# Kernel optimization log

Measured on AMD Instinct MI355X. Metric: run time of the kernel, lower is better.

The kernel has to match this reference:

```python
import jax, jax.numpy as jnp
import numpy as np

B, T, DIM, S, DFF = 4, 2048, 2048, 4, 8192
SINKHORN_ITERS = 10


def setup_inputs() -> dict:
    key = jax.random.key(0)
    ks = jax.random.split(key, 12)

    def lin(k, fan_in, shape):
        bound = 1.0 / np.sqrt(fan_in)
        return jax.random.uniform(k, shape, jnp.float32, -bound, bound)

    return {
        "x": jax.random.normal(ks[0], (B, T, DIM), jnp.float32),
        # phi_* linears act on the S-times tiled vector of size S*DIM
        "phi_pre_w": lin(ks[1], S * DIM, (S, S * DIM)),
        "phi_pre_b": lin(ks[2], S * DIM, (S,)),
        "phi_post_w": lin(ks[3], S * DIM, (S, S * DIM)),
        "phi_post_b": lin(ks[4], S * DIM, (S,)),
        "phi_res_w": lin(ks[5], S * DIM, (S * S, S * DIM)),
        "phi_res_b": lin(ks[6], S * DIM, (S * S,)),
        "alpha_pre": jnp.ones((1,), jnp.float32),
        "alpha_post": jnp.ones((1,), jnp.float32),
        "alpha_res": jnp.ones((1,), jnp.float32),
        "b_pre": jnp.zeros((S,), jnp.float32),
        "b_post": jnp.zeros((S,), jnp.float32),
        "b_res": jnp.zeros((S, S), jnp.float32),
        # block = transformer MLP
        "W1": lin(ks[7], DIM, (DIM, DFF)),
        "b1": lin(ks[8], DIM, (DFF,)),
        "W2": lin(ks[9], DFF, (DFF, DIM)),
        "b2": lin(ks[10], DFF, (DIM,)),
    }


def sinkhorn_knopp(logits):
    # logits: [B, T, S, S] -> doubly-stochastic via exp + alternating normalization
    M = jnp.exp(logits)
    for _ in range(SINKHORN_ITERS):
        M = M / jnp.sum(M, axis=-1, keepdims=True)  # rows
        M = M / jnp.sum(M, axis=-2, keepdims=True)  # cols
    return M


def reference(x, phi_pre_w, phi_pre_b, phi_post_w, phi_post_b, phi_res_w,
              phi_res_b, alpha_pre, alpha_post, alpha_res, b_pre, b_post,
              b_res, W1, b1, W2, b2):
    bs, seq, d = x.shape
    s = b_pre.shape[0]
    eps = jnp.asarray(jnp.finfo(x.dtype).eps, x.dtype)
    # x_l = x expanded over S identical streams; x_vec = tile(x, S).
    # RMS over the tiled S*d vector == RMS over d (streams are copies).
    x_n = x * jax.lax.rsqrt(jnp.mean(x * x, axis=-1, keepdims=True) + eps)
    # Linear on the tiled vector == sum of the S weight blocks applied to x_n.
    Wp = phi_pre_w.reshape(s, s, d).sum(axis=1)        # [S, d]
    Wq = phi_post_w.reshape(s, s, d).sum(axis=1)       # [S, d]
    Wr = phi_res_w.reshape(s * s, s, d).sum(axis=1)    # [S*S, d]
    h_pre_t = alpha_pre * (jnp.einsum('btd,sd->bts', x_n, Wp) + phi_pre_b) + b_pre
    h_post_t = alpha_post * (jnp.einsum('btd,sd->bts', x_n, Wq) + phi_post_b) + b_post
    h_res_t = alpha_res * (jnp.einsum('btd,kd->btk', x_n, Wr) + phi_res_b)
    h_res_t = h_res_t.reshape(bs, seq, s, s) + b_res
    h_pre = jax.nn.sigmoid(h_pre_t)                    # [B,T,S]
    h_post = 2.0 * jax.nn.sigmoid(h_post_t)            # [B,T,S]
    h_res = sinkhorn_knopp(h_res_t)                    # [B,T,S,S]
    # block_input = sum_j x_l[:,:,j] * h_pre[...,j] ; streams identical -> x * sum_j h_pre
    block_input = x * jnp.sum(h_pre, axis=-1, keepdims=True)
    # block: MLP with exact (erf) GELU, matching torch default
    h = jax.nn.gelu(jnp.einsum('btd,df->btf', block_input, W1) + b1, approximate=False)
    block_out = jnp.einsum('btf,fd->btd', h, W2) + b2
    # out = sum_i [ (h_res @ x_l)_i + h_post_i * block_out ]
    #     = x * sum_{ij} h_res[ij] + block_out * sum_i h_post_i
    res_mix = jnp.sum(h_res, axis=(-2, -1))[..., None]         # [B,T,1]
    post_mix = jnp.sum(h_post, axis=-1, keepdims=True)          # [B,T,1]
    return x * res_mix + block_out * post_mix
```

## Files before the change

kernel.cpp:

```cpp
#include <hip/hip_runtime.h>
#include <hip/hip_bf16.h>
#include <cstdint>
#include <cstddef>

#define DIM   2048
#define DFF   8192
#define NROWS 8192
#define NFOLD 24

typedef float f32x4 __attribute__((ext_vector_type(4)));
typedef __bf16 bf16x8 __attribute__((ext_vector_type(8)));

__device__ __forceinline__ float sigmoidf_(float v) { return 1.0f / (1.0f + expf(-v)); }

__device__ __forceinline__ unsigned short f2bf(float v) {
    union { __hip_bfloat16 h; unsigned short u; } cv;
    cv.h = __float2bfloat16(v);
    return cv.u;
}

__device__ __forceinline__ void async_copy16(const void* g, void* l) {
    __builtin_amdgcn_global_load_lds((const __attribute__((address_space(1))) void*)g,
                                     (__attribute__((address_space(3))) void*)l, 16, 0, 0);
}

__device__ __forceinline__ void wg_barrier() {
    asm volatile("" ::: "memory");
    __builtin_amdgcn_s_barrier();
    asm volatile("" ::: "memory");
}

#define VM(n) asm volatile("s_waitcnt vmcnt(" #n ")" ::: "memory")
#define LGKM0 asm volatile("s_waitcnt lgkmcnt(0)" ::: "memory")

__global__ __launch_bounds__(256) void fold_kernel(const float* __restrict__ pre_w,
                                                   const float* __restrict__ post_w,
                                                   const float* __restrict__ res_w,
                                                   float* __restrict__ Wfold) {
    int idx = blockIdx.x * 256 + threadIdx.x;
    if (idx >= NFOLD * DIM) return;
    int r = idx >> 11;
    int d = idx & (DIM - 1);
    const float* src;
    if (r < 4)      src = pre_w  + (size_t)r * (4 * DIM);
    else if (r < 8) src = post_w + (size_t)(r - 4) * (4 * DIM);
    else            src = res_w  + (size_t)(r - 8) * (4 * DIM);
    Wfold[idx] = src[d] + src[DIM + d] + src[2 * DIM + d] + src[3 * DIM + d];
}

__global__ __launch_bounds__(256) void transpose_to_bf16(const float* __restrict__ in,
                                                         __hip_bfloat16* __restrict__ out,
                                                         int R, int C) {
    __shared__ float tile[32][33];
    int bx = blockIdx.x, by = blockIdx.y;
    int tx = threadIdx.x & 31, ty0 = threadIdx.x >> 5;
#pragma unroll
    for (int i = 0; i < 4; i++) {
        int ty = ty0 + i * 8;
        tile[ty][tx] = in[(size_t)(by * 32 + ty) * C + bx * 32 + tx];
    }
    __syncthreads();
#pragma unroll
    for (int i = 0; i < 4; i++) {
        int ty = ty0 + i * 8;
        out[(size_t)(bx * 32 + ty) * R + by * 32 + tx] = __float2bfloat16(tile[tx][ty]);
    }
}

__global__ __launch_bounds__(512) void gating_kernel(
    const float* __restrict__ x, const float* __restrict__ Wfold,
    const float* __restrict__ phi_pre_b, const float* __restrict__ phi_post_b,
    const float* __restrict__ phi_res_b,
    const float* __restrict__ alpha_pre, const float* __restrict__ alpha_post,
    const float* __restrict__ alpha_res,
    const float* __restrict__ b_pre, const float* __restrict__ b_post,
    const float* __restrict__ b_res,
    __hip_bfloat16* __restrict__ Abuf,
    float* __restrict__ g_res_arr, float* __restrict__ g_post_arr) {
    const int tid = threadIdx.x;
    const int lane = tid & 63, wave = tid >> 6;
    const int row = blockIdx.x * 8 + wave;

    const float4* x4 = (const float4*)x + (size_t)row * 512;
    const float4* w4 = (const float4*)Wfold;

    float4 xv[8];
#pragma unroll
    for (int j = 0; j < 8; j++) xv[j] = x4[j * 64 + lane];

    float p[25];
    p[24] = 0.f;
#pragma unroll
    for (int j = 0; j < 8; j++)
        p[24] += xv[j].x * xv[j].x + xv[j].y * xv[j].y + xv[j].z * xv[j].z + xv[j].w * xv[j].w;

    for (int r = 0; r < NFOLD; r++) {
        float acc = 0.f;
#pragma unroll
        for (int j = 0; j < 8; j++) {
            float4 wv = w4[r * 512 + j * 64 + lane];
            acc += xv[j].x * wv.x + xv[j].y * wv.y + xv[j].z * wv.z + xv[j].w * wv.w;
        }
        p[r] = acc;
    }

#pragma unroll
    for (int r = 0; r < 25; r++) {
        float v = p[r];
#pragma unroll
        for (int off = 1; off < 64; off <<= 1) v += __shfl_xor(v, off, 64);
        p[r] = v;
    }

    const float rms = rsqrtf(p[24] / (float)DIM + 1.1920928955078125e-07f);
    const float ap = alpha_pre[0], aq = alpha_post[0], ar = alpha_res[0];
    float gpre = 0.f, gpost = 0.f;
#pragma unroll
    for (int s = 0; s < 4; s++) {
        gpre  += sigmoidf_(ap * (rms * p[s]     + phi_pre_b[s])  + b_pre[s]);
        gpost += 2.0f * sigmoidf_(aq * (rms * p[4 + s] + phi_post_b[s]) + b_post[s]);
    }
    float Mm[4][4];
#pragma unroll
    for (int i = 0; i < 4; i++)
#pragma unroll
        for (int j = 0; j < 4; j++) {
            int k = i * 4 + j;
            Mm[i][j] = expf(ar * (rms * p[8 + k] + phi_res_b[k]) + b_res[k]);
        }
    for (int it = 0; it < 10; ++it) {
#pragma unroll
        for (int i = 0; i < 4; i++) {
            float rs = 1.0f / (Mm[i][0] + Mm[i][1] + Mm[i][2] + Mm[i][3]);
#pragma unroll
            for (int j = 0; j < 4; j++) Mm[i][j] *= rs;
        }
#pragma unroll
        for (int j = 0; j < 4; j++) {
            float cs = 1.0f / (Mm[0][j] + Mm[1][j] + Mm[2][j] + Mm[3][j]);
#pragma unroll
            for (int i = 0; i < 4; i++) Mm[i][j] *= cs;
        }
    }
    float gres = 0.f;
#pragma unroll
    for (int i = 0; i < 4; i++)
#pragma unroll
        for (int j = 0; j < 4; j++) gres += Mm[i][j];

    __hip_bfloat16* arow = Abuf + (size_t)row * DIM;
#pragma unroll
    for (int j = 0; j < 8; j++) {
        ushort4 u;
        u.x = f2bf(xv[j].x * gpre); u.y = f2bf(xv[j].y * gpre);
        u.z = f2bf(xv[j].z * gpre); u.w = f2bf(xv[j].w * gpre);
        *reinterpret_cast<ushort4*>(arow + (j * 64 + lane) * 4) = u;
    }
    if (lane == 0) {
        g_res_arr[row]  = gres;
        g_post_arr[row] = gpost;
    }
}

#define RD_A0                                                                     \
    _Pragma("unroll") for (int m = 0; m < 4; ++m) {                               \
        a0[m][0] = *(const bf16x8*)(A0r + baseA + m * 2048 + cb0);                \
        a0[m][1] = *(const bf16x8*)(A0r + baseA + m * 2048 + cb1);                \
    }
#define RD_A1                                                                     \
    _Pragma("unroll") for (int m = 0; m < 4; ++m) {                               \
        a1[m][0] = *(const bf16x8*)(A1r + baseA + m * 2048 + cb0);                \
        a1[m][1] = *(const bf16x8*)(A1r + baseA + m * 2048 + cb1);                \
    }
#define RD_B0                                                                     \
    _Pragma("unroll") for (int n = 0; n < 2; ++n) {                               \
        b0[n][0] = *(const bf16x8*)(B0r + baseB + n * 2048 + cb0);                \
        b0[n][1] = *(const bf16x8*)(B0r + baseB + n * 2048 + cb1);                \
    }
#define RD_B1                                                                     \
    _Pragma("unroll") for (int n = 0; n < 2; ++n) {                               \
        b1[n][0] = *(const bf16x8*)(B1r + baseB + n * 2048 + cb0);                \
        b1[n][1] = *(const bf16x8*)(B1r + baseB + n * 2048 + cb1);                \
    }

#define MQ(AF, BF, MO, NO)                                                        \
    __builtin_amdgcn_s_setprio(1);                                                \
    _Pragma("unroll") for (int m = 0; m < 4; ++m)                                 \
    _Pragma("unroll") for (int n = 0; n < 2; ++n) {                               \
        acc[(MO) + m][(NO) + n] = __builtin_amdgcn_mfma_f32_16x16x32_bf16(        \
            AF[m][0], BF[n][0], acc[(MO) + m][(NO) + n], 0, 0, 0);                \
        acc[(MO) + m][(NO) + n] = __builtin_amdgcn_mfma_f32_16x16x32_bf16(        \
            AF[m][1], BF[n][1], acc[(MO) + m][(NO) + n], 0, 0, 0);                \
    }                                                                             \
    __builtin_amdgcn_s_setprio(0);

#define STG_A(t_, h_)                                                             \
    if ((t_) < nk) {                                                              \
        char* l_ = ldsA + (((t_) & 1) * 32768) + (h_) * 16384 + wave * 1024;      \
        async_copy16(Ab + aOff[0][h_] + (size_t)(t_) * 128, l_);                  \
        async_copy16(Ab + aOff[1][h_] + (size_t)(t_) * 128, l_ + 8192);           \
    }
#define STG_B(t_, h_)                                                             \
    if ((t_) < nk) {                                                              \
        char* l_ = ldsB + (((t_) & 1) * 32768) + (h_) * 16384 + wave * 1024;      \
        async_copy16(Bb + bOff[0][h_] + (size_t)(t_) * 128, l_);                  \
        async_copy16(Bb + bOff[1][h_] + (size_t)(t_) * 128, l_ + 8192);           \
    }

template <int MODE, int NB>
__global__ __launch_bounds__(512, 2) void gemm256(
    const __hip_bfloat16* __restrict__ A, const __hip_bfloat16* __restrict__ Bt,
    int M, int N, int K, const float* __restrict__ bias,
    __hip_bfloat16* __restrict__ outh, float* __restrict__ outf,
    const float* __restrict__ x, const float* __restrict__ g_res,
    const float* __restrict__ g_post) {
    __shared__ __align__(16) char ldsA[65536];
    __shared__ __align__(16) char ldsB[65536];

    const int wg = blockIdx.x;
    const int xcd = wg & 7;
    const int i = wg >> 3;
    const int nt = xcd * NB + (i % NB);
    const int mt = i / NB;
    const int m0 = mt * 256;
    const int n0 = nt * 256;

    const int tid = threadIdx.x;
    const int lane = tid & 63;
    const int wave = tid >> 6;
    const int wr = wave >> 2;
    const int wc = wave & 3;
    const int q = lane >> 4;
    const int rr = lane & 7;

    const uint32_t cb0 = (uint32_t)((q ^ rr) << 4);
    const uint32_t cb1 = (uint32_t)(((4 + q) ^ rr) << 4);
    const uint32_t baseA = (uint32_t)((wr * 64 + (lane & 15)) * 128);
    const uint32_t baseB = (uint32_t)((wc * 32 + (lane & 15)) * 128);

    const uint32_t scb = (uint32_t)((((lane & 7) ^ ((lane >> 3) & 7))) << 4);
    const int lr = lane >> 3;
    const size_t K2 = (size_t)K * 2;
    size_t aOff[2][2], bOff[2][2];
#pragma unroll
    for (int ii = 0; ii < 2; ++ii)
#pragma unroll
        for (int h = 0; h < 2; ++h) {
            int gA = m0 + wave * 8 + lr + ii * 128 + h * 64;
            int gB = n0 + ((wave >> 2) + 2 * ii) * 64 + h * 32 + (wave & 3) * 8 + lr;
            aOff[ii][h] = (size_t)gA * K2 + scb;
            bOff[ii][h] = (size_t)gB * K2 + scb;
        }
    const char* Ab = (const char*)A;
    const char* Bb = (const char*)Bt;

    f32x4 acc[8][4];
#pragma unroll
    for (int m = 0; m < 8; ++m)
#pragma unroll
        for (int n = 0; n < 4; ++n) acc[m][n] = (f32x4){0.f, 0.f, 0.f, 0.f};

    const int nk = K / 64;

    STG_A(0, 0); STG_B(0, 0); STG_B(0, 1); STG_A(0, 1);
    STG_A(1, 0); STG_B(1, 0); STG_B(1, 1); STG_A(1, 1);
    VM(12);
    wg_barrier();

    bf16x8 a0[4][2], a1[4][2];
    bf16x8 b0[2][2], b1[2][2];

    for (int kt = 0; kt < nk; ++kt) {
        const int c = kt & 1;
        const char* A0r = ldsA + c * 32768;
        const char* A1r = A0r + 16384;
        const char* B0r = ldsB + c * 32768;
        const char* B1r = B0r + 16384;
        RD_A0
        RD_B0
        if (kt + 1 < nk) { VM(10); } else { VM(2); }
        wg_barrier();
        MQ(a0, b0, 0, 0)
        LGKM0;
        wg_barrier();
        RD_B1
        STG_A(kt + 2, 0); STG_B(kt + 2, 0);
        if (kt + 2 < nk) { VM(12); } else if (kt + 1 < nk) { VM(8); } else { VM(0); }
        wg_barrier();
        MQ(a0, b1, 0, 2)
        LGKM0;
        wg_barrier();
        RD_A1
        STG_B(kt + 2, 1);
        wg_barrier();
        MQ(a1, b0, 4, 0)
        LGKM0;
        wg_barrier();
        STG_A(kt + 2, 1);
        if (kt + 2 < nk) {
            VM(12);
            wg_barrier();
        } else if (kt + 1 < nk) {
            VM(4);
            wg_barrier();
        }
        MQ(a1, b1, 4, 2)
    }

#pragma unroll
    for (int mi = 0; mi < 8; ++mi) {
#pragma unroll
        for (int ni = 0; ni < 4; ++ni) {
            const int col = n0 + wc * 64 + (ni >> 1) * 32 + (ni & 1) * 16 + (lane & 15);
            const float bc = bias[col];
#pragma unroll
            for (int j = 0; j < 4; ++j) {
                const int row = m0 + wr * 128 + (mi >> 2) * 64 + (mi & 3) * 16 + q * 4 + j;
                float v = acc[mi][ni][j] + bc;
                if (MODE == 1) {
                    float u = 1.5957691216057308f * (v + 0.044715f * v * v * v);
                    float s = 1.0f / (1.0f + __expf(-u));
                    outh[(size_t)row * N + col] = __float2bfloat16(v * s);
                } else {
                    outf[(size_t)row * N + col] =
                        x[(size_t)row * N + col] * g_res[row] + v * g_post[row];
                }
            }
        }
    }
}

extern "C" void kernel_launch(void* const* d_in, const int* in_sizes, int n_in,
                              void* d_out, int out_size, void* d_ws, size_t ws_size,
                              hipStream_t stream) {
    const float* x          = (const float*)d_in[0];
    const float* phi_pre_w  = (const float*)d_in[1];
    const float* phi_pre_b  = (const float*)d_in[2];
    const float* phi_post_w = (const float*)d_in[3];
    const float* phi_post_b = (const float*)d_in[4];
    const float* phi_res_w  = (const float*)d_in[5];
    const float* phi_res_b  = (const float*)d_in[6];
    const float* alpha_pre  = (const float*)d_in[7];
    const float* alpha_post = (const float*)d_in[8];
    const float* alpha_res  = (const float*)d_in[9];
    const float* b_pre      = (const float*)d_in[10];
    const float* b_post     = (const float*)d_in[11];
    const float* b_res      = (const float*)d_in[12];
    const float* W1         = (const float*)d_in[13];
    const float* b1         = (const float*)d_in[14];
    const float* W2         = (const float*)d_in[15];
    const float* b2         = (const float*)d_in[16];
    float* out = (float*)d_out;

    char* ws = (char*)d_ws;
    __hip_bfloat16* W1T  = (__hip_bfloat16*)ws;
    __hip_bfloat16* W2T  = W1T + (size_t)DFF * DIM;
    __hip_bfloat16* Abuf = W2T + (size_t)DIM * DFF;
    __hip_bfloat16* Hbuf = Abuf + (size_t)NROWS * DIM;
    float* Wfold = (float*)(Hbuf + (size_t)NROWS * DFF);
    float* gres  = Wfold + NFOLD * DIM;
    float* gpost = gres + NROWS;

    fold_kernel<<<(NFOLD * DIM + 255) / 256, 256, 0, stream>>>(phi_pre_w, phi_post_w,
                                                               phi_res_w, Wfold);
    transpose_to_bf16<<<dim3(DFF / 32, DIM / 32), 256, 0, stream>>>(W1, W1T, DIM, DFF);
    transpose_to_bf16<<<dim3(DIM / 32, DFF / 32), 256, 0, stream>>>(W2, W2T, DFF, DIM);
    gating_kernel<<<NROWS / 8, 512, 0, stream>>>(x, Wfold, phi_pre_b, phi_post_b, phi_res_b,
                                                 alpha_pre, alpha_post, alpha_res,
                                                 b_pre, b_post, b_res, Abuf, gres, gpost);
    gemm256<1, 4><<<1024, 512, 0, stream>>>(
        Abuf, W1T, NROWS, DFF, DIM, b1, Hbuf, nullptr, nullptr, nullptr, nullptr);
    gemm256<2, 1><<<256, 512, 0, stream>>>(
        Hbuf, W2T, NROWS, DIM, DFF, b2, nullptr, out, x, gres, gpost);
}
```

Baseline: 721.1 us.

## Software-pipeline LDS fragment reads ahead of MFMA quarters in GEMM main loop

Restructures the GEMM k-loop so that each MFMA quarter overlaps with the LDS reads for the next quarter's fragments and with the next global-to-LDS async stage. The first A0/B0 fragments are preloaded before the loop, and the next tile's a0/b0 are prefetched at the end of each iteration. This replaces the read-then-barrier-then-compute sequence, aiming to hide LDS latency behind matrix instructions. The vmcnt wait thresholds are re-tuned for the new issue order, which risks correctness or stalls if the counts are wrong.

```diff
diff --git a/kernel.cpp b/kernel.cpp
--- a/kernel.cpp
+++ b/kernel.cpp
@@ -162,25 +162,15 @@
     }
 }
 
-#define RD_A0                                                                     \
+#define RD_A(DST, REG)                                                            \
     _Pragma("unroll") for (int m = 0; m < 4; ++m) {                               \
-        a0[m][0] = *(const bf16x8*)(A0r + baseA + m * 2048 + cb0);                \
-        a0[m][1] = *(const bf16x8*)(A0r + baseA + m * 2048 + cb1);                \
-    }
-#define RD_A1                                                                     \
-    _Pragma("unroll") for (int m = 0; m < 4; ++m) {                               \
-        a1[m][0] = *(const bf16x8*)(A1r + baseA + m * 2048 + cb0);                \
-        a1[m][1] = *(const bf16x8*)(A1r + baseA + m * 2048 + cb1);                \
-    }
-#define RD_B0                                                                     \
+        DST[m][0] = *(const bf16x8*)((REG) + baseA + m * 2048 + cb0);             \
+        DST[m][1] = *(const bf16x8*)((REG) + baseA + m * 2048 + cb1);             \
+    }
+#define RD_B(DST, REG)                                                            \
     _Pragma("unroll") for (int n = 0; n < 2; ++n) {                               \
-        b0[n][0] = *(const bf16x8*)(B0r + baseB + n * 2048 + cb0);                \
-        b0[n][1] = *(const bf16x8*)(B0r + baseB + n * 2048 + cb1);                \
-    }
-#define RD_B1                                                                     \
-    _Pragma("unroll") for (int n = 0; n < 2; ++n) {                               \
-        b1[n][0] = *(const bf16x8*)(B1r + baseB + n * 2048 + cb0);                \
-        b1[n][1] = *(const bf16x8*)(B1r + baseB + n * 2048 + cb1);                \
+        DST[n][0] = *(const bf16x8*)((REG) + baseB + n * 2048 + cb0);             \
+        DST[n][1] = *(const bf16x8*)((REG) + baseB + n * 2048 + cb1);             \
     }
 
 #define MQ(AF, BF, MO, NO)                                                        \
@@ -262,49 +252,50 @@
 
     const int nk = K / 64;
 
-    STG_A(0, 0); STG_B(0, 0); STG_B(0, 1); STG_A(0, 1);
-    STG_A(1, 0); STG_B(1, 0); STG_B(1, 1); STG_A(1, 1);
-    VM(12);
+    STG_A(0, 0); STG_B(0, 0); STG_A(0, 1); STG_B(0, 1);
+    STG_A(1, 0); STG_B(1, 0); STG_A(1, 1); STG_B(1, 1);
+    VM(8);
     wg_barrier();
 
     bf16x8 a0[4][2], a1[4][2];
     bf16x8 b0[2][2], b1[2][2];
+    RD_A(a0, ldsA)
+    RD_B(b0, ldsB)
+    LGKM0;
+    wg_barrier();
 
     for (int kt = 0; kt < nk; ++kt) {
         const int c = kt & 1;
-        const char* A0r = ldsA + c * 32768;
-        const char* A1r = A0r + 16384;
-        const char* B0r = ldsB + c * 32768;
-        const char* B1r = B0r + 16384;
-        RD_A0
-        RD_B0
-        if (kt + 1 < nk) { VM(10); } else { VM(2); }
-        wg_barrier();
+        const int cn = c ^ 1;
+        const char* Ac = ldsA + c * 32768;
+        const char* Bc = ldsB + c * 32768;
+        const char* An = ldsA + cn * 32768;
+        const char* Bn = ldsB + cn * 32768;
+        const bool steady = (kt < nk - 2);
+        RD_B(b1, Bc + 16384)
+        STG_A(kt + 2, 0)
         MQ(a0, b0, 0, 0)
         LGKM0;
+        if (steady) { VM(12); } else { VM(0); }
         wg_barrier();
-        RD_B1
-        STG_A(kt + 2, 0); STG_B(kt + 2, 0);
-        if (kt + 2 < nk) { VM(12); } else if (kt + 1 < nk) { VM(8); } else { VM(0); }
-        wg_barrier();
+        RD_A(a1, Ac + 16384)
+        STG_B(kt + 2, 0)
         MQ(a0, b1, 0, 2)
         LGKM0;
+        if (steady) { VM(10); } else { VM(0); }
         wg_barrier();
-        RD_A1
-        STG_B(kt + 2, 1);
-        wg_barrier();
+        if (kt + 1 < nk) { RD_A(a0, An) }
+        STG_A(kt + 2, 1)
         MQ(a1, b0, 4, 0)
         LGKM0;
+        if (steady) { VM(10); } else { VM(0); }
         wg_barrier();
-        STG_A(kt + 2, 1);
-        if (kt + 2 < nk) {
-            VM(12);
-            wg_barrier();
-        } else if (kt + 1 < nk) {
-            VM(4);
-            wg_barrier();
-        }
+        if (kt + 1 < nk) { RD_B(b0, Bn) }
+        STG_B(kt + 2, 1)
         MQ(a1, b1, 4, 2)
+        LGKM0;
+        if (steady) { VM(8); } else { VM(0); }
+        wg_barrier();
     }
 
 #pragma unroll
```

After: 690.3 us. -4.3%, faster.
